# Kernel tuning notes

Measured on AMD Instinct MI355X. Metric: run time of the kernel, lower is better.

Reference implementation:

```python
import jax, jax.numpy as jnp
import numpy as np

MARGIN = 0.075
CONF_THRESHOLD = 0.2


def setup_inputs() -> dict:
    key = jax.random.key(0)
    k1, k2, k3 = jax.random.split(key, 3)
    N, D = 32768, 256
    embeddings = jax.random.normal(k1, (N, D), dtype=jnp.float32)
    tags = jax.random.randint(k2, (N,), 0, 500, dtype=jnp.int64)
    confidences = jax.random.uniform(k3, (N,), dtype=jnp.float32)
    return {"embeddings": embeddings, "tags": tags, "confidences": confidences}


def _safe_sqrt(sq):
    # gradient-safe sqrt: zero at sq<=0 (matches d(0)=0, avoids NaN in vjp)
    pos = sq > 0
    return jnp.where(pos, jnp.sqrt(jnp.where(pos, sq, 1.0)), 0.0)


def _triplet_hard_mining(emb, labels):
    n = emb.shape[0]
    # pairwise euclidean distances (cdist p=2)
    sq_norm = jnp.sum(emb * emb, axis=1)  # [n]
    sq = sq_norm[:, None] + sq_norm[None, :] - 2.0 * (emb @ emb.T)
    dist = _safe_sqrt(jnp.maximum(sq, 0.0))  # [n, n]

    same = labels[:, None] == labels[None, :]
    eye = jnp.eye(n, dtype=bool)
    pos_mask = same & ~eye
    neg_mask = ~same

    inf = jnp.float32(jnp.inf)
    hard_pos = jnp.max(jnp.where(pos_mask, dist, -inf), axis=1)  # [n]
    neg_min = jnp.min(jnp.where(neg_mask, dist, inf), axis=1)    # [n]
    # semi-hard negatives: neg dists strictly greater than hardest positive
    shn_mask = neg_mask & (dist > hard_pos[:, None])
    shn_min = jnp.min(jnp.where(shn_mask, dist, inf), axis=1)
    hard_neg = jnp.where(jnp.isfinite(shn_min), shn_min, neg_min)

    valid = jnp.any(pos_mask, axis=1) & jnp.any(neg_mask, axis=1)
    per_anchor = jax.nn.relu(hard_pos - hard_neg + MARGIN)
    per_anchor = jnp.where(valid, per_anchor, 0.0)
    cnt = jnp.sum(valid.astype(jnp.float32))
    # if no valid anchors (also covers <2 unique labels), loss is 0
    return jnp.where(cnt > 0, jnp.sum(per_anchor) / jnp.maximum(cnt, 1.0), 0.0)


def reference(embeddings, tags, confidences):
    n = embeddings.shape[0]
    top_k = int(CONF_THRESHOLD * n)
    _, idx = jax.lax.top_k(confidences, top_k)
    emb = embeddings[idx]
    labels = tags[idx]
    return _triplet_hard_mining(emb, labels)
```

## Files before the change

kernel.cpp:

```cpp
#include <hip/hip_runtime.h>
#include <math.h>

#define D 256
#define MARGIN 0.075f
#define MAXM 96
#define NBIN 16384

typedef __bf16 bf8_t __attribute__((ext_vector_type(8)));
typedef float f4_t __attribute__((ext_vector_type(4)));
typedef unsigned long long ull;

#define AS1 __attribute__((address_space(1)))
#define AS3 __attribute__((address_space(3)))
static __device__ __forceinline__ void gload_lds16(const void* g, void* s) {
    __builtin_amdgcn_global_load_lds((const AS1 unsigned int*)g, (AS3 unsigned int*)s, 16, 0, 0);
}

#define ALOADU(p) __hip_atomic_load((p), __ATOMIC_RELAXED, __HIP_MEMORY_SCOPE_AGENT)
#define ASTOREU(p, v) __hip_atomic_store((p), (v), __ATOMIC_RELAXED, __HIP_MEMORY_SCOPE_AGENT)

#define VDRAIN() asm volatile("s_waitcnt vmcnt(0)" ::: "memory")

static __device__ __forceinline__ unsigned short f2bf(float x) {
    unsigned u = __float_as_uint(x);
    unsigned r = (u + 0x7fffu + ((u >> 16) & 1u)) >> 16;
    return (unsigned short)r;
}

static __device__ __forceinline__ float dec_min(unsigned cm) {
    return (cm == 0u) ? __builtin_inff() : __uint_as_float(~cm);
}

static __device__ __forceinline__ float rmin16(float v) {
    int s;
    s = __builtin_amdgcn_update_dpp(__float_as_int(v), __float_as_int(v), 0x101, 0xF, 0xF, false);
    v = fminf(v, __int_as_float(s));
    s = __builtin_amdgcn_update_dpp(__float_as_int(v), __float_as_int(v), 0x102, 0xF, 0xF, false);
    v = fminf(v, __int_as_float(s));
    s = __builtin_amdgcn_update_dpp(__float_as_int(v), __float_as_int(v), 0x104, 0xF, 0xF, false);
    v = fminf(v, __int_as_float(s));
    s = __builtin_amdgcn_update_dpp(__float_as_int(v), __float_as_int(v), 0x108, 0xF, 0xF, false);
    v = fminf(v, __int_as_float(s));
    return v;
}

__global__ __launch_bounds__(1024) void k_hist(const float* __restrict__ conf, int n,
                                               unsigned* __restrict__ hist,
                                               unsigned* __restrict__ ctrl, int ksel) {
    int t = threadIdx.x;
    int i = blockIdx.x * 1024 + t;
    if (i < n) {
        unsigned b = __float_as_uint(conf[i]) >> 16;
        if (b > NBIN - 1u) b = NBIN - 1u;
        atomicAdd(&hist[b], 1u);
    }
    VDRAIN();
    __syncthreads();
    __shared__ int lastf;
    if (t == 0) lastf = (atomicAdd(&ctrl[10], 1u) == gridDim.x - 1) ? 1 : 0;
    __syncthreads();
    if (!lastf) return;

    __shared__ unsigned part[1024];
    __shared__ int schunk;
    unsigned k = (unsigned)ksel;
    unsigned loc[16];
    unsigned s = 0;
    #pragma unroll
    for (int b = 0; b < 16; b++) {
        loc[b] = ALOADU(&hist[t * 16 + b]);
        s += loc[b];
    }
    part[t] = s;
    __syncthreads();
    for (int off = 1; off < 1024; off <<= 1) {
        unsigned v = (t + off < 1024) ? part[t + off] : 0u;
        __syncthreads();
        part[t] += v;
        __syncthreads();
    }
    if (part[t] >= k && (t == 1023 || part[t + 1] < k)) schunk = t;
    __syncthreads();
    int c = schunk;
    if (t == c) {
        unsigned cum = (c == 1023) ? 0u : part[c + 1];
        int bin = 0; unsigned rem = 1;
        #pragma unroll
        for (int b = 15; b >= 0; b--) {
            unsigned h = loc[b];
            if (cum + h >= k) { bin = c * 16 + b; rem = k - cum; break; }
            cum += h;
        }
        ctrl[3] = (unsigned)bin;
        ctrl[1] = k - rem;
        ctrl[2] = rem;
    }
}

__global__ __launch_bounds__(1024) void k_sel(const float* __restrict__ conf, int n,
                                              unsigned* __restrict__ ctrl,
                                              int* __restrict__ idx_sel,
                                              ull* __restrict__ cand) {
    int t = threadIdx.x;
    int i = blockIdx.x * 1024 + t;
    unsigned b16 = ctrl[3];
    if (i < n) {
        unsigned u = __float_as_uint(conf[i]);
        unsigned t16 = u >> 16;
        if (t16 > NBIN - 1u) t16 = NBIN - 1u;
        if (t16 > b16) {
            unsigned pos = atomicAdd(&ctrl[5], 1u);
            idx_sel[pos] = i;
        } else if (t16 == b16) {
            unsigned pos = atomicAdd(&ctrl[6], 1u);
            ASTOREU(&cand[pos], ((ull)u << 32) | (unsigned)i);
        }
    }
    VDRAIN();
    __syncthreads();
    __shared__ int lastf;
    if (t == 0) lastf = (atomicAdd(&ctrl[11], 1u) == gridDim.x - 1) ? 1 : 0;
    __syncthreads();
    if (!lastf) return;

    __shared__ ull scand[2048];
    int M = (int)ALOADU(&ctrl[6]);
    unsigned need = ctrl[2], cgt = ctrl[1];
    if (M <= 2048) {
        for (int j = t; j < M; j += 1024) scand[j] = ALOADU(&cand[j]);
        __syncthreads();
        for (int j = t; j < M; j += 1024) {
            ull cj = scand[j];
            unsigned uj = (unsigned)(cj >> 32);
            unsigned rank = 0;
            for (int m = 0; m < M; m++) {
                ull cm = scand[m];
                unsigned um = (unsigned)(cm >> 32);
                if (um > uj || (um == uj && cm < cj)) rank++;
            }
            if (rank < need) idx_sel[cgt + rank] = (int)(unsigned)(cj & 0xFFFFFFFFu);
        }
    } else {
        for (int j = t; j < M; j += 1024) {
            ull cj = ALOADU(&cand[j]);
            unsigned uj = (unsigned)(cj >> 32);
            unsigned rank = 0;
            for (int m = 0; m < M; m++) {
                ull cm = ALOADU(&cand[m]);
                unsigned um = (unsigned)(cm >> 32);
                if (um > uj || (um == uj && cm < cj)) rank++;
            }
            if (rank < need) idx_sel[cgt + rank] = (int)(unsigned)(cj & 0xFFFFFFFFu);
        }
    }
}

__global__ __launch_bounds__(256) void k_gather(const float* __restrict__ emb,
                                                const int* __restrict__ tags,
                                                const int* __restrict__ idx_sel,
                                                int ksel, int np,
                                                unsigned short* __restrict__ ebf,
                                                float* __restrict__ sqn,
                                                int* __restrict__ lsel,
                                                unsigned* __restrict__ labhist,
                                                int* __restrict__ members) {
    int j = blockIdx.x * 4 + (threadIdx.x >> 6);
    int t = threadIdx.x & 63;
    if (j < ksel) {
        int src = idx_sel[j];
        float4 v = *(const float4*)&emb[(size_t)src * D + t * 4];
        ushort4 o;
        o.x = f2bf(v.x); o.y = f2bf(v.y); o.z = f2bf(v.z); o.w = f2bf(v.w);
        *(ushort4*)&ebf[(size_t)j * D + t * 4] = o;
        float s = v.x * v.x + v.y * v.y + v.z * v.z + v.w * v.w;
        for (int off = 32; off > 0; off >>= 1) s += __shfl_down(s, off);
        if (t == 0) {
            int lab = tags[src];
            sqn[j] = s; lsel[j] = lab;
            unsigned slot = atomicAdd(&labhist[lab], 1u);
            if (slot < MAXM) members[lab * MAXM + slot] = j;
        }
    } else if (j < np) {
        ushort4 z = {0, 0, 0, 0};
        *(ushort4*)&ebf[(size_t)j * D + t * 4] = z;
        if (t == 0) { sqn[j] = __builtin_inff(); lsel[j] = -1; }
    }
}

__global__ __launch_bounds__(256) void k_hardpos(const unsigned short* __restrict__ ebf,
                                                 const float* __restrict__ sqn,
                                                 const int* __restrict__ members,
                                                 const unsigned* __restrict__ labhist,
                                                 unsigned* __restrict__ hp_g) {
    int L = blockIdx.x;
    int t = threadIdx.x;
    int m = (int)labhist[L];
    if (m > MAXM) m = MAXM;
    if (m < 2) return;

    __shared__ unsigned short rows[MAXM * 256];
    __shared__ float lsqn[MAXM];
    __shared__ unsigned hpl[MAXM];
    __shared__ int ridx[MAXM];

    for (int a = t; a < m; a += 256) {
        int r = members[L * MAXM + a];
        ridx[a] = r; lsqn[a] = sqn[r]; hpl[a] = 0u;
    }
    __syncthreads();
    for (int e = t * 8; e < m * 256; e += 256 * 8) {
        int a = e >> 8, c = e & 255;
        *(uint4*)&rows[a * 256 + c] = *(const uint4*)&ebf[(size_t)ridx[a] * D + c];
    }
    __syncthreads();

    int npair = m * (m - 1) / 2;
    for (int pidx = t; pidx < npair; pidx += 256) {
        int a = 0, rem = pidx;
        while (rem >= m - 1 - a) { rem -= m - 1 - a; a++; }
        int b = a + 1 + rem;
        const unsigned* ra = (const unsigned*)&rows[a * 256];
        const unsigned* rb = (const unsigned*)&rows[b * 256];
        float dot = 0.f;
        #pragma unroll 8
        for (int c = 0; c < 128; c++) {
            unsigned ua = ra[c], ub = rb[c];
            float a0 = __uint_as_float(ua << 16);
            float a1 = __uint_as_float(ua & 0xFFFF0000u);
            float b0 = __uint_as_float(ub << 16);
            float b1 = __uint_as_float(ub & 0xFFFF0000u);
            dot = fmaf(a0, b0, dot);
            dot = fmaf(a1, b1, dot);
        }
        float dsq = fmaxf(lsqn[a] + lsqn[b] - 2.f * dot, 0.f);
        unsigned bits = __float_as_uint(dsq);
        atomicMax(&hpl[a], bits);
        atomicMax(&hpl[b], bits);
    }
    __syncthreads();
    for (int a = t; a < m; a += 256) hp_g[ridx[a]] = hpl[a];
}

__global__ __launch_bounds__(256, 3) void k_fused(const unsigned short* __restrict__ Ebf,
                                                  const float* __restrict__ sqn,
                                                  const int* __restrict__ lsel,
                                                  const unsigned* __restrict__ hp_g,
                                                  unsigned* __restrict__ nm_g,
                                                  unsigned* __restrict__ shn_g,
                                                  int np, int nb, int ksel) {
    int rem = blockIdx.x, bi = 0;
    while (rem >= nb - bi) { rem -= nb - bi; bi++; }
    int bj = bi + rem;
    int i0 = bi * 128, j0 = bj * 128;
    bool diag = (bi == bj);

    __shared__ __align__(16) char smem[32768];
    char* ldsA = smem;
    char* ldsB = smem + 16384;

    int t = threadIdx.x;
    int w = t >> 6, l = t & 63;
    int wm = w & 1, wn = w >> 1;
    int lr = l & 15, lq = l >> 4;
    int r7 = lr & 7, rh = lr >> 3;

    int dr = l >> 3;
    int sg = (l & 7) ^ dr;
    const unsigned short* gA = Ebf + (size_t)(i0 + dr) * D + sg * 8;
    const unsigned short* gB = Ebf + (size_t)(j0 + dr) * D + sg * 8;

    f4_t zero = {0.f, 0.f, 0.f, 0.f};
    f4_t acc[4][4];
    #pragma unroll
    for (int p = 0; p < 4; p++)
        #pragma unroll
        for (int q = 0; q < 4; q++) acc[p][q] = zero;

    for (int k0 = 0; k0 < D; k0 += 64) {
        #pragma unroll
        for (int c = 0; c < 4; c++) {
            int R0 = w * 32 + c * 8;
            gload_lds16(gA + (size_t)R0 * D + k0, ldsA + R0 * 128);
            gload_lds16(gB + (size_t)R0 * D + k0, ldsB + R0 * 128);
        }
        __syncthreads();
        #pragma unroll
        for (int ks8 = 0; ks8 < 8; ks8 += 4) {
            bf8_t a[4], b[4];
            #pragma unroll
            for (int p = 0; p < 4; p++) {
                int off = ((wm * 8 + p * 2 + rh) << 10) + ((r7 * 8 + ((ks8 + lq) ^ r7)) << 4);
                a[p] = *(const bf8_t*)(ldsA + off);
            }
            #pragma unroll
            for (int q = 0; q < 4; q++) {
                int off = ((wn * 8 + q * 2 + rh) << 10) + ((r7 * 8 + ((ks8 + lq) ^ r7)) << 4);
                b[q] = *(const bf8_t*)(ldsB + off);
            }
            #pragma unroll
            for (int p = 0; p < 4; p++)
                #pragma unroll
                for (int q = 0; q < 4; q++)
                    acc[p][q] = __builtin_amdgcn_mfma_f32_16x16x32_bf16(a[p], b[q], acc[p][q], 0, 0, 0);
        }
        __syncthreads();
    }

    float* sqnA = (float*)smem;
    float* sqnB = sqnA + 128;
    int* labA = (int*)(sqnB + 128);
    int* labB = labA + 128;
    float* hpA2 = (float*)(labB + 128);
    float* hpB2 = hpA2 + 128;
    if (t < 128) {
        sqnA[t] = sqn[i0 + t];
        labA[t] = lsel[i0 + t];
        hpA2[t] = __uint_as_float(hp_g[i0 + t]);
    } else {
        int u = t - 128;
        sqnB[u] = sqn[j0 + u];
        labB[u] = lsel[j0 + u];
        hpB2[u] = __uint_as_float(hp_g[j0 + u]);
    }
    __syncthreads();

    const float INF = __builtin_inff();
    float dsq[4][4][4];
    int colL[4], ljv[4];
    float sBv[4];
    #pragma unroll
    for (int q = 0; q < 4; q++) {
        colL[q] = wn * 64 + q * 16 + lr;
        ljv[q] = labB[colL[q]];
        sBv[q] = sqnB[colL[q]];
    }
    #pragma unroll
    for (int p = 0; p < 4; p++) {
        #pragma unroll
        for (int r = 0; r < 4; r++) {
            int rowL = wm * 64 + p * 16 + lq * 4 + r;
            float smi = sqnA[rowL];
            #pragma unroll
            for (int q = 0; q < 4; q++)
                dsq[p][q][r] = fmaxf(smi + sBv[q] - 2.f * acc[p][q][r], 0.f);
        }
    }

    #pragma unroll
    for (int p = 0; p < 4; p++) {
        #pragma unroll
        for (int r = 0; r < 4; r++) {
            int rowL = wm * 64 + p * 16 + lq * 4 + r;
            int li = labA[rowL];
            float hpr = hpA2[rowL];
            float nmv = INF, smv = INF;
            #pragma unroll
            for (int q = 0; q < 4; q++) {
                float d = dsq[p][q][r];
                if (ljv[q] != li) {
                    nmv = fminf(nmv, d);
                    if (d > hpr) smv = fminf(smv, d);
                }
            }
            nmv = rmin16(nmv);
            smv = rmin16(smv);
            if (lr == 0) {
                if (nmv < INF) atomicMax(&nm_g[i0 + rowL], ~__float_as_uint(nmv));
                if (smv < INF) atomicMax(&shn_g[i0 + rowL], ~__float_as_uint(smv));
            }
        }
    }

    if (!diag) {
        #pragma unroll
        for (int q = 0; q < 4; q++) {
            int lj = ljv[q];
            float hpc = hpB2[colL[q]];
            float nmv = INF, smv = INF;
            #pragma unroll
            for (int p = 0; p < 4; p++)
                #pragma unroll
                for (int r = 0; r < 4; r++) {
                    int rowL = wm * 64 + p * 16 + lq * 4 + r;
                    float d = dsq[p][q][r];
                    if (labA[rowL] != lj) {
                        nmv = fminf(nmv, d);
                        if (d > hpc) smv = fminf(smv, d);
                    }
                }
            nmv = fminf(nmv, __shfl_xor(nmv, 16));
            nmv = fminf(nmv, __shfl_xor(nmv, 32));
            smv = fminf(smv, __shfl_xor(smv, 16));
            smv = fminf(smv, __shfl_xor(smv, 32));
            if (lq == 0) {
                if (nmv < INF) atomicMax(&nm_g[j0 + colL[q]], ~__float_as_uint(nmv));
                if (smv < INF) atomicMax(&shn_g[j0 + colL[q]], ~__float_as_uint(smv));
            }
        }
    }
}

__global__ __launch_bounds__(256) void k_loss(const unsigned* __restrict__ hp,
                                              const unsigned* __restrict__ nm,
                                              const unsigned* __restrict__ shn,
                                              const int* __restrict__ lsel,
                                              const unsigned* __restrict__ labhist,
                                              int ksel, float* __restrict__ fsums,
                                              unsigned* __restrict__ ctrl,
                                              float* __restrict__ out) {
    __shared__ float ssum[256], scnt[256];
    int t = threadIdx.x;
    int i = blockIdx.x * 256 + t;
    float sum = 0.f, cnt = 0.f;
    if (i < ksel) {
        int li = lsel[i];
        unsigned h = labhist[li];
        bool valid = (h >= 2u) && ((unsigned)ksel > h);
        if (valid) {
            float hp2 = __uint_as_float(hp[i]);
            float nm2 = dec_min(nm[i]);
            float sh2 = dec_min(shn[i]);
            float hn2 = isinf(sh2) ? nm2 : sh2;
            sum = fmaxf(sqrtf(hp2) - sqrtf(hn2) + MARGIN, 0.f);
            cnt = 1.f;
        }
    }
    ssum[t] = sum; scnt[t] = cnt;
    __syncthreads();
    for (int off = 128; off > 0; off >>= 1) {
        if (t < off) { ssum[t] += ssum[t + off]; scnt[t] += scnt[t + off]; }
        __syncthreads();
    }
    if (t == 0) {
        atomicAdd(&fsums[0], ssum[0]);
        atomicAdd(&fsums[1], scnt[0]);
        VDRAIN();
        unsigned done = atomicAdd(&ctrl[7], 1u);
        if (done == gridDim.x - 1) {
            float s = atomicAdd(&fsums[0], 0.f);
            float c = atomicAdd(&fsums[1], 0.f);
            out[0] = (c > 0.f) ? (s / fmaxf(c, 1.f)) : 0.f;
        }
    }
}

__global__ void k_wsfail(float* out, float code) { out[0] = code; }

static inline size_t align_up(size_t x, size_t a) { return (x + a - 1) & ~(a - 1); }

extern "C" void kernel_launch(void* const* d_in, const int* in_sizes, int n_in,
                              void* d_out, int out_size, void* d_ws, size_t ws_size,
                              hipStream_t stream) {
    const float* emb  = (const float*)d_in[0];
    const int*   tags = (const int*)d_in[1];
    const float* conf = (const float*)d_in[2];
    float* out = (float*)d_out;

    int n = in_sizes[2];
    int ksel = (int)(0.2 * (double)n);
    int np = ((ksel + 127) / 128) * 128;
    int nb = np / 128;
    int nlab = 512;

    size_t off = 0;
    size_t o_ctrl = off; off = align_up(off + 32 * sizeof(unsigned), 256);
    size_t o_fs   = off; off = align_up(off + 8 * sizeof(float), 256);
    size_t o_lh   = off; off = align_up(off + (size_t)nlab * 4, 256);
    size_t o_hp   = off; off = align_up(off + (size_t)np * 4, 256);
    size_t o_nm   = off; off = align_up(off + (size_t)np * 4, 256);
    size_t o_shn  = off; off = align_up(off + (size_t)np * 4, 256);
    size_t o_h1   = off; off = align_up(off + (size_t)NBIN * 4, 256);
    size_t zero_bytes = off;
    size_t o_idx  = off; off = align_up(off + (size_t)ksel * 4, 256);
    size_t o_cand = off; off = align_up(off + (size_t)n * 8, 256);
    size_t o_mem  = off; off = align_up(off + (size_t)nlab * MAXM * 4, 256);
    size_t o_lab  = off; off = align_up(off + (size_t)np * 4, 256);
    size_t o_sqn  = off; off = align_up(off + (size_t)np * 4, 256);
    size_t o_ebf  = off; off = align_up(off + (size_t)np * D * 2, 256);

    if (ws_size < off) {
        k_wsfail<<<1, 1, 0, stream>>>(out, -(float)(ws_size >> 20));
        return;
    }

    char* ws = (char*)d_ws;
    unsigned*       ctrl    = (unsigned*)(ws + o_ctrl);
    float*          fsums   = (float*)(ws + o_fs);
    unsigned*       labhist = (unsigned*)(ws + o_lh);
    unsigned*       hp_g    = (unsigned*)(ws + o_hp);
    unsigned*       nm_g    = (unsigned*)(ws + o_nm);
    unsigned*       shn_g   = (unsigned*)(ws + o_shn);
    unsigned*       h1      = (unsigned*)(ws + o_h1);
    int*            idx_sel = (int*)(ws + o_idx);
    ull*            cand    = (ull*)(ws + o_cand);
    int*            members = (int*)(ws + o_mem);
    int*            lsel    = (int*)(ws + o_lab);
    float*          sqn     = (float*)(ws + o_sqn);
    unsigned short* ebf     = (unsigned short*)(ws + o_ebf);

    hipMemsetAsync(d_ws, 0, zero_bytes, stream);
    int nhb = (n + 1023) / 1024;
    k_hist<<<nhb, 1024, 0, stream>>>(conf, n, h1, ctrl, ksel);
    k_sel<<<nhb, 1024, 0, stream>>>(conf, n, ctrl, idx_sel, cand);
    k_gather<<<np / 4, 256, 0, stream>>>(emb, tags, idx_sel, ksel, np, ebf, sqn, lsel,
                                         labhist, members);
    k_hardpos<<<512, 256, 0, stream>>>(ebf, sqn, members, labhist, hp_g);
    int ntri = nb * (nb + 1) / 2;
    k_fused<<<ntri, 256, 0, stream>>>(ebf, sqn, lsel, hp_g, nm_g, shn_g, np, nb, ksel);
    k_loss<<<(ksel + 255) / 256, 256, 0, stream>>>(hp_g, nm_g, shn_g, lsel, labhist,
                                                   ksel, fsums, ctrl, out);
}
```

Baseline: 181.2 us.

## Fuse histogram/select and gather/hardpos kernels using in-kernel grid barriers

Merges the histogram and selection kernels into one launch, with a spin-wait flag published by the last block. Also merges the gather and hard-positive kernels, using a grid-stride gather followed by an atomic-counter grid barrier. The goal is to cut two kernel launches and their inter-kernel gaps. The spin barriers assume all blocks are co-resident (32 blocks of 1024 threads, and nlab blocks of 256 with large LDS), otherwise they can deadlock. The atomic relaxed loads and stores add memory traffic overhead.

```diff
diff --git a/kernel.cpp b/kernel.cpp
--- a/kernel.cpp
+++ b/kernel.cpp
@@ -44,70 +44,72 @@
     return v;
 }
 
-__global__ __launch_bounds__(1024) void k_hist(const float* __restrict__ conf, int n,
-                                               unsigned* __restrict__ hist,
-                                               unsigned* __restrict__ ctrl, int ksel) {
+__global__ __launch_bounds__(1024) void k_histsel(const float* __restrict__ conf, int n,
+                                                  unsigned* __restrict__ hist,
+                                                  unsigned* __restrict__ ctrl, int ksel,
+                                                  int* __restrict__ idx_sel,
+                                                  ull* __restrict__ cand) {
     int t = threadIdx.x;
     int i = blockIdx.x * 1024 + t;
+    unsigned u = 0, t16 = 0;
     if (i < n) {
-        unsigned b = __float_as_uint(conf[i]) >> 16;
-        if (b > NBIN - 1u) b = NBIN - 1u;
-        atomicAdd(&hist[b], 1u);
+        u = __float_as_uint(conf[i]);
+        t16 = u >> 16;
+        if (t16 > NBIN - 1u) t16 = NBIN - 1u;
+        atomicAdd(&hist[t16], 1u);
     }
     VDRAIN();
     __syncthreads();
     __shared__ int lastf;
     if (t == 0) lastf = (atomicAdd(&ctrl[10], 1u) == gridDim.x - 1) ? 1 : 0;
     __syncthreads();
-    if (!lastf) return;
-
-    __shared__ unsigned part[1024];
-    __shared__ int schunk;
-    unsigned k = (unsigned)ksel;
-    unsigned loc[16];
-    unsigned s = 0;
-    #pragma unroll
-    for (int b = 0; b < 16; b++) {
-        loc[b] = ALOADU(&hist[t * 16 + b]);
-        s += loc[b];
-    }
-    part[t] = s;
-    __syncthreads();
-    for (int off = 1; off < 1024; off <<= 1) {
-        unsigned v = (t + off < 1024) ? part[t + off] : 0u;
+
+    if (lastf) {
+        __shared__ unsigned part[1024];
+        __shared__ int schunk;
+        unsigned k = (unsigned)ksel;
+        unsigned loc[16];
+        unsigned s = 0;
+        #pragma unroll
+        for (int b = 0; b < 16; b++) {
+            loc[b] = ALOADU(&hist[t * 16 + b]);
+            s += loc[b];
+        }
+        part[t] = s;
         __syncthreads();
-        part[t] += v;
+        for (int off = 1; off < 1024; off <<= 1) {
+            unsigned v = (t + off < 1024) ? part[t + off] : 0u;
+            __syncthreads();
+            part[t] += v;
+            __syncthreads();
+        }
+        if (part[t] >= k && (t == 1023 || part[t + 1] < k)) schunk = t;
         __syncthreads();
-    }
-    if (part[t] >= k && (t == 1023 || part[t + 1] < k)) schunk = t;
-    __syncthreads();
-    int c = schunk;
-    if (t == c) {
-        unsigned cum = (c == 1023) ? 0u : part[c + 1];
-        int bin = 0; unsigned rem = 1;
-        #pragma unroll
-        for (int b = 15; b >= 0; b--) {
-            unsigned h = loc[b];
-            if (cum + h >= k) { bin = c * 16 + b; rem = k - cum; break; }
-            cum += h;
-        }
-        ctrl[3] = (unsigned)bin;
-        ctrl[1] = k - rem;
-        ctrl[2] = rem;
-    }
-}
-
-__global__ __launch_bounds__(1024) void k_sel(const float* __restrict__ conf, int n,
-                                              unsigned* __restrict__ ctrl,
-                                              int* __restrict__ idx_sel,
-                                              ull* __restrict__ cand) {
-    int t = threadIdx.x;
-    int i = blockIdx.x * 1024 + t;
-    unsigned b16 = ctrl[3];
+        int c = schunk;
+        if (t == c) {
+            unsigned cum = (c == 1023) ? 0u : part[c + 1];
+            int bin = 0; unsigned rem = 1;
+            #pragma unroll
+            for (int b = 15; b >= 0; b--) {
+                unsigned h = loc[b];
+                if (cum + h >= k) { bin = c * 16 + b; rem = k - cum; break; }
+                cum += h;
+            }
+            ASTOREU(&ctrl[3], (unsigned)bin);
+            ASTOREU(&ctrl[1], k - rem);
+            ASTOREU(&ctrl[2], rem);
+            VDRAIN();
+            ASTOREU(&ctrl[14], 1u);
+        }
+    }
+
+    if (t == 0) {
+        while (ALOADU(&ctrl[14]) == 0u) __builtin_amdgcn_s_sleep(2);
+    }
+    __syncthreads();
+    unsigned b16 = ALOADU(&ctrl[3]);
+
     if (i < n) {
-        unsigned u = __float_as_uint(conf[i]);
-        unsigned t16 = u >> 16;
-        if (t16 > NBIN - 1u) t16 = NBIN - 1u;
         if (t16 > b16) {
             unsigned pos = atomicAdd(&ctrl[5], 1u);
             idx_sel[pos] = i;
@@ -118,14 +120,14 @@
     }
     VDRAIN();
     __syncthreads();
-    __shared__ int lastf;
-    if (t == 0) lastf = (atomicAdd(&ctrl[11], 1u) == gridDim.x - 1) ? 1 : 0;
-    __syncthreads();
-    if (!lastf) return;
+    __shared__ int lastf2;
+    if (t == 0) lastf2 = (atomicAdd(&ctrl[11], 1u) == gridDim.x - 1) ? 1 : 0;
+    __syncthreads();
+    if (!lastf2) return;
 
     __shared__ ull scand[2048];
     int M = (int)ALOADU(&ctrl[6]);
-    unsigned need = ctrl[2], cgt = ctrl[1];
+    unsigned need = ALOADU(&ctrl[2]), cgt = ALOADU(&ctrl[1]);
     if (M <= 2048) {
         for (int j = t; j < M; j += 1024) scand[j] = ALOADU(&cand[j]);
         __syncthreads();
@@ -155,46 +157,55 @@
     }
 }
 
-__global__ __launch_bounds__(256) void k_gather(const float* __restrict__ emb,
-                                                const int* __restrict__ tags,
-                                                const int* __restrict__ idx_sel,
-                                                int ksel, int np,
-                                                unsigned short* __restrict__ ebf,
-                                                float* __restrict__ sqn,
-                                                int* __restrict__ lsel,
-                                                unsigned* __restrict__ labhist,
-                                                int* __restrict__ members) {
-    int j = blockIdx.x * 4 + (threadIdx.x >> 6);
-    int t = threadIdx.x & 63;
-    if (j < ksel) {
-        int src = idx_sel[j];
-        float4 v = *(const float4*)&emb[(size_t)src * D + t * 4];
-        ushort4 o;
-        o.x = f2bf(v.x); o.y = f2bf(v.y); o.z = f2bf(v.z); o.w = f2bf(v.w);
-        *(ushort4*)&ebf[(size_t)j * D + t * 4] = o;
-        float s = v.x * v.x + v.y * v.y + v.z * v.z + v.w * v.w;
-        for (int off = 32; off > 0; off >>= 1) s += __shfl_down(s, off);
-        if (t == 0) {
-            int lab = tags[src];
-            sqn[j] = s; lsel[j] = lab;
-            unsigned slot = atomicAdd(&labhist[lab], 1u);
-            if (slot < MAXM) members[lab * MAXM + slot] = j;
-        }
-    } else if (j < np) {
-        ushort4 z = {0, 0, 0, 0};
-        *(ushort4*)&ebf[(size_t)j * D + t * 4] = z;
-        if (t == 0) { sqn[j] = __builtin_inff(); lsel[j] = -1; }
-    }
-}
-
-__global__ __launch_bounds__(256) void k_hardpos(const unsigned short* __restrict__ ebf,
-                                                 const float* __restrict__ sqn,
-                                                 const int* __restrict__ members,
-                                                 const unsigned* __restrict__ labhist,
-                                                 unsigned* __restrict__ hp_g) {
+__global__ __launch_bounds__(256) void k_gatherpos(const float* __restrict__ emb,
+                                                   const int* __restrict__ tags,
+                                                   const int* __restrict__ idx_sel,
+                                                   int ksel, int np,
+                                                   unsigned short* __restrict__ ebf,
+                                                   float* __restrict__ sqn,
+                                                   int* __restrict__ lsel,
+                                                   unsigned* __restrict__ labhist,
+                                                   int* __restrict__ members,
+                                                   unsigned* __restrict__ hp_g,
+                                                   unsigned* __restrict__ ctrl) {
+    int t = threadIdx.x;
+    int ngrp = np / 4;
+    for (int g = blockIdx.x; g < ngrp; g += gridDim.x) {
+        int j = g * 4 + (t >> 6);
+        int lane = t & 63;
+        if (j < ksel) {
+            int src = idx_sel[j];
+            float4 v = *(const float4*)&emb[(size_t)src * D + lane * 4];
+            ull pk = (ull)f2bf(v.x) | ((ull)f2bf(v.y) << 16) |
+                     ((ull)f2bf(v.z) << 32) | ((ull)f2bf(v.w) << 48);
+            ASTOREU((ull*)&ebf[(size_t)j * D + lane * 4], pk);
+            float s = v.x * v.x + v.y * v.y + v.z * v.z + v.w * v.w;
+            for (int off = 32; off > 0; off >>= 1) s += __shfl_down(s, off);
+            if (lane == 0) {
+                int lab = tags[src];
+                ASTOREU((unsigned*)&sqn[j], __float_as_uint(s));
+                lsel[j] = lab;
+                unsigned slot = atomicAdd(&labhist[lab], 1u);
+                if (slot < MAXM) ASTOREU((unsigned*)&members[lab * MAXM + slot], (unsigned)j);
+            }
+        } else {
+            ASTOREU((ull*)&ebf[(size_t)j * D + lane * 4], 0ull);
+            if (lane == 0) {
+                ASTOREU((unsigned*)&sqn[j], __float_as_uint(__builtin_inff()));
+                lsel[j] = -1;
+            }
+        }
+    }
+    VDRAIN();
+    __syncthreads();
+    if (t == 0) {
+        if (atomicAdd(&ctrl[12], 1u) == gridDim.x - 1) ASTOREU(&ctrl[13], 1u);
+        while (ALOADU(&ctrl[13]) == 0u) __builtin_amdgcn_s_sleep(2);
+    }
+    __syncthreads();
+
     int L = blockIdx.x;
-    int t = threadIdx.x;
-    int m = (int)labhist[L];
+    int m = (int)ALOADU(&labhist[L]);
     if (m > MAXM) m = MAXM;
     if (m < 2) return;
 
@@ -204,13 +215,18 @@
     __shared__ int ridx[MAXM];
 
     for (int a = t; a < m; a += 256) {
-        int r = members[L * MAXM + a];
-        ridx[a] = r; lsqn[a] = sqn[r]; hpl[a] = 0u;
+        int r = (int)ALOADU((unsigned*)&members[L * MAXM + a]);
+        ridx[a] = r;
+        lsqn[a] = __uint_as_float(ALOADU((unsigned*)&sqn[r]));
+        hpl[a] = 0u;
     }
     __syncthreads();
     for (int e = t * 8; e < m * 256; e += 256 * 8) {
         int a = e >> 8, c = e & 255;
-        *(uint4*)&rows[a * 256 + c] = *(const uint4*)&ebf[(size_t)ridx[a] * D + c];
+        ull lo = ALOADU((ull*)&ebf[(size_t)ridx[a] * D + c]);
+        ull hi = ALOADU((ull*)&ebf[(size_t)ridx[a] * D + c + 4]);
+        *(ull*)&rows[a * 256 + c] = lo;
+        *(ull*)&rows[a * 256 + c + 4] = hi;
     }
     __syncthreads();
 
@@ -500,11 +516,9 @@
 
     hipMemsetAsync(d_ws, 0, zero_bytes, stream);
     int nhb = (n + 1023) / 1024;
-    k_hist<<<nhb, 1024, 0, stream>>>(conf, n, h1, ctrl, ksel);
-    k_sel<<<nhb, 1024, 0, stream>>>(conf, n, ctrl, idx_sel, cand);
-    k_gather<<<np / 4, 256, 0, stream>>>(emb, tags, idx_sel, ksel, np, ebf, sqn, lsel,
-                                         labhist, members);
-    k_hardpos<<<512, 256, 0, stream>>>(ebf, sqn, members, labhist, hp_g);
+    k_histsel<<<nhb, 1024, 0, stream>>>(conf, n, h1, ctrl, ksel, idx_sel, cand);
+    k_gatherpos<<<nlab, 256, 0, stream>>>(emb, tags, idx_sel, ksel, np, ebf, sqn,
+                                          lsel, labhist, members, hp_g, ctrl);
     int ntri = nb * (nb + 1) / 2;
     k_fused<<<ntri, 256, 0, stream>>>(ebf, sqn, lsel, hp_g, nm_g, shn_g, np, nb, ksel);
     k_loss<<<(ksel + 255) / 256, 256, 0, stream>>>(hp_g, nm_g, shn_g, lsel, labhist,
```

Measured after the change: 198.6 us. 1.1x slower.

## Fuse histogram and selection kernels with per-block redundant LDS histogram

Applied to the files above, without the earlier changes.

Merges the top-k histogram and selection kernels into a single launch. Every block now builds the full confidence histogram in shared memory by reading all n confidences, so no global histogram or last-block handoff is needed before selection. The bin count drops to 8192 (shift by 17) so the histogram fits in LDS alongside scratch space. This removes a kernel launch and a global atomic histogram pass, at the cost of each block redundantly scanning all confidences and possibly larger boundary-bin candidate sets.

```diff
diff --git a/kernel.cpp b/kernel.cpp
--- a/kernel.cpp
+++ b/kernel.cpp
@@ -4,7 +4,7 @@
 #define D 256
 #define MARGIN 0.075f
 #define MAXM 96
-#define NBIN 16384
+#define NBIN 8192
 
 typedef __bf16 bf8_t __attribute__((ext_vector_type(8)));
 typedef float f4_t __attribute__((ext_vector_type(4)));
@@ -20,6 +20,7 @@
 #define ASTOREU(p, v) __hip_atomic_store((p), (v), __ATOMIC_RELAXED, __HIP_MEMORY_SCOPE_AGENT)
 
 #define VDRAIN() asm volatile("s_waitcnt vmcnt(0)" ::: "memory")
+
 
 static __device__ __forceinline__ unsigned short f2bf(float x) {
     unsigned u = __float_as_uint(x);
@@ -44,33 +45,29 @@
     return v;
 }
 
-__global__ __launch_bounds__(1024) void k_hist(const float* __restrict__ conf, int n,
-                                               unsigned* __restrict__ hist,
-                                               unsigned* __restrict__ ctrl, int ksel) {
+__global__ __launch_bounds__(1024) void k_histsel(const float* __restrict__ conf, int n,
+                                                  unsigned* __restrict__ ctrl, int ksel,
+                                                  int* __restrict__ idx_sel,
+                                                  ull* __restrict__ cand) {
+    __shared__ __align__(16) unsigned shist[NBIN];
+    __shared__ __align__(16) char aux[16384];
+    unsigned* part = (unsigned*)aux;
     int t = threadIdx.x;
-    int i = blockIdx.x * 1024 + t;
-    if (i < n) {
-        unsigned b = __float_as_uint(conf[i]) >> 16;
+
+    for (int b = t; b < NBIN; b += 1024) shist[b] = 0u;
+    __syncthreads();
+    for (int i = t; i < n; i += 1024) {
+        unsigned b = __float_as_uint(conf[i]) >> 17;
         if (b > NBIN - 1u) b = NBIN - 1u;
-        atomicAdd(&hist[b], 1u);
-    }
-    VDRAIN();
-    __syncthreads();
-    __shared__ int lastf;
-    if (t == 0) lastf = (atomicAdd(&ctrl[10], 1u) == gridDim.x - 1) ? 1 : 0;
-    __syncthreads();
-    if (!lastf) return;
-
-    __shared__ unsigned part[1024];
-    __shared__ int schunk;
+        atomicAdd(&shist[b], 1u);
+    }
+    __syncthreads();
+
     unsigned k = (unsigned)ksel;
-    unsigned loc[16];
+    unsigned loc[8];
     unsigned s = 0;
     #pragma unroll
-    for (int b = 0; b < 16; b++) {
-        loc[b] = ALOADU(&hist[t * 16 + b]);
-        s += loc[b];
-    }
+    for (int b = 0; b < 8; b++) { loc[b] = shist[t * 8 + b]; s += loc[b]; }
     part[t] = s;
     __syncthreads();
     for (int off = 1; off < 1024; off <<= 1) {
@@ -79,6 +76,8 @@
         part[t] += v;
         __syncthreads();
     }
+    __shared__ int schunk;
+    __shared__ unsigned sbin, sneed, scgt;
     if (part[t] >= k && (t == 1023 || part[t + 1] < k)) schunk = t;
     __syncthreads();
     int c = schunk;
@@ -86,32 +85,25 @@
         unsigned cum = (c == 1023) ? 0u : part[c + 1];
         int bin = 0; unsigned rem = 1;
         #pragma unroll
-        for (int b = 15; b >= 0; b--) {
+        for (int b = 7; b >= 0; b--) {
             unsigned h = loc[b];
-            if (cum + h >= k) { bin = c * 16 + b; rem = k - cum; break; }
+            if (cum + h >= k) { bin = c * 8 + b; rem = k - cum; break; }
             cum += h;
         }
-        ctrl[3] = (unsigned)bin;
-        ctrl[1] = k - rem;
-        ctrl[2] = rem;
-    }
-}
-
-__global__ __launch_bounds__(1024) void k_sel(const float* __restrict__ conf, int n,
-                                              unsigned* __restrict__ ctrl,
-                                              int* __restrict__ idx_sel,
-                                              ull* __restrict__ cand) {
-    int t = threadIdx.x;
+        sbin = (unsigned)bin; sneed = rem; scgt = k - rem;
+    }
+    __syncthreads();
+    unsigned b16 = sbin, need = sneed, cgt = scgt;
+
     int i = blockIdx.x * 1024 + t;
-    unsigned b16 = ctrl[3];
     if (i < n) {
         unsigned u = __float_as_uint(conf[i]);
-        unsigned t16 = u >> 16;
-        if (t16 > NBIN - 1u) t16 = NBIN - 1u;
-        if (t16 > b16) {
+        unsigned tb = u >> 17;
+        if (tb > NBIN - 1u) tb = NBIN - 1u;
+        if (tb > b16) {
             unsigned pos = atomicAdd(&ctrl[5], 1u);
             idx_sel[pos] = i;
-        } else if (t16 == b16) {
+        } else if (tb == b16) {
             unsigned pos = atomicAdd(&ctrl[6], 1u);
             ASTOREU(&cand[pos], ((ull)u << 32) | (unsigned)i);
         }
@@ -123,9 +115,8 @@
     __syncthreads();
     if (!lastf) return;
 
-    __shared__ ull scand[2048];
-    int M = (int)ALOADU(&ctrl[6]);
-    unsigned need = ctrl[2], cgt = ctrl[1];
+    ull* scand = (ull*)aux;
+    int M = (int)atomicAdd(&ctrl[6], 0u);
     if (M <= 2048) {
         for (int j = t; j < M; j += 1024) scand[j] = ALOADU(&cand[j]);
         __syncthreads();
@@ -469,7 +460,6 @@
     size_t o_hp   = off; off = align_up(off + (size_t)np * 4, 256);
     size_t o_nm   = off; off = align_up(off + (size_t)np * 4, 256);
     size_t o_shn  = off; off = align_up(off + (size_t)np * 4, 256);
-    size_t o_h1   = off; off = align_up(off + (size_t)NBIN * 4, 256);
     size_t zero_bytes = off;
     size_t o_idx  = off; off = align_up(off + (size_t)ksel * 4, 256);
     size_t o_cand = off; off = align_up(off + (size_t)n * 8, 256);
@@ -490,7 +480,6 @@
     unsigned*       hp_g    = (unsigned*)(ws + o_hp);
     unsigned*       nm_g    = (unsigned*)(ws + o_nm);
     unsigned*       shn_g   = (unsigned*)(ws + o_shn);
-    unsigned*       h1      = (unsigned*)(ws + o_h1);
     int*            idx_sel = (int*)(ws + o_idx);
     ull*            cand    = (ull*)(ws + o_cand);
     int*            members = (int*)(ws + o_mem);
@@ -500,8 +489,7 @@
 
     hipMemsetAsync(d_ws, 0, zero_bytes, stream);
     int nhb = (n + 1023) / 1024;
-    k_hist<<<nhb, 1024, 0, stream>>>(conf, n, h1, ctrl, ksel);
-    k_sel<<<nhb, 1024, 0, stream>>>(conf, n, ctrl, idx_sel, cand);
+    k_histsel<<<nhb, 1024, 0, stream>>>(conf, n, ctrl, ksel, idx_sel, cand);
     k_gather<<<np / 4, 256, 0, stream>>>(emb, tags, idx_sel, ksel, np, ebf, sqn, lsel,
                                          labhist, members);
     k_hardpos<<<512, 256, 0, stream>>>(ebf, sqn, members, labhist, hp_g);
```

Result: faster. 172.6 us (median of 2 runs) (-4.8%).
